# Performance work log

Hardware: AMD Instinct MI355X
Metric: run time of the kernel (lower is better)

The kernel has to match this reference:

```python
import jax, jax.numpy as jnp
import numpy as np

H = 32  # hidden/input size fixed by the module

def _rnn_layer(x, W_ih, b_ih, W_hh, b_hh):
    # x: [B, T, H]. PyTorch RNN: h_t = tanh(x_t @ W_ih^T + b_ih + h_{t-1} @ W_hh^T + b_hh)
    B = x.shape[0]
    # precompute input projection for all timesteps (one big GEMM)
    xin = jnp.einsum('bth,ih->bti', x, W_ih) + (b_ih + b_hh)  # [B, T, H]
    def step(h, xt):
        h_new = jnp.tanh(xt + h @ W_hh.T)
        return h_new, h_new
    h0 = jnp.zeros((B, H), dtype=x.dtype)
    _, hs = jax.lax.scan(step, h0, jnp.swapaxes(xin, 0, 1))  # hs: [T, B, H]
    return jnp.swapaxes(hs, 0, 1)  # [B, T, H]


def setup_inputs() -> dict:
    key = jax.random.key(0)
    ks = jax.random.split(key, 11)
    s = 1.0 / np.sqrt(H)
    u = lambda k, shape: jax.random.uniform(k, shape, jnp.float32, -s, s)
    x = jax.random.normal(ks[0], (4096, 512, H), dtype=jnp.float32)
    return {
        'x': x,
        'W_ih1': u(ks[1], (H, H)), 'W_hh1': u(ks[2], (H, H)),
        'b_ih1': u(ks[3], (H,)),   'b_hh1': u(ks[4], (H,)),
        'W_ih2': u(ks[5], (H, H)), 'W_hh2': u(ks[6], (H, H)),
        'b_ih2': u(ks[7], (H,)),   'b_hh2': u(ks[8], (H,)),
        'W_fc': u(ks[9], (1, H)),  'b_fc': u(ks[10], (1,)),
    }


def reference(x, W_ih1, W_hh1, b_ih1, b_hh1, W_ih2, W_hh2, b_ih2, b_hh2, W_fc, b_fc):
    h1 = _rnn_layer(x, W_ih1, b_ih1, W_hh1, b_hh1)   # [B, T, H]
    h2 = _rnn_layer(h1, W_ih2, b_ih2, W_hh2, b_hh2)  # [B, T, H]
    last = h2[:, -1, :]                               # [B, H]
    return last @ W_fc.T + b_fc                       # [B, 1]
```

## Files before the change

### kernel.cpp

```cpp
#include <hip/hip_runtime.h>

#define HH 32
#define TT 512
#define CHUNK 8
#define NCHUNK (TT / CHUNK)

__device__ __forceinline__ float fast_tanh(float z) {
    float e, r;
    float zz = z * 2.88539008177793f;
    asm("v_exp_f32 %0, %1" : "=v"(e) : "v"(zz));
    float d = e + 1.0f;
    asm("v_rcp_f32 %0, %1" : "=v"(r) : "v"(d));
    return __builtin_fmaf(-2.0f, r, 1.0f);
}

__global__ void __launch_bounds__(64) __attribute__((amdgpu_waves_per_eu(2, 2)))
rnn_fused(
    const float* __restrict__ x,
    const float* __restrict__ Wih1, const float* __restrict__ Whh1,
    const float* __restrict__ bih1, const float* __restrict__ bhh1,
    const float* __restrict__ Wih2, const float* __restrict__ Whh2,
    const float* __restrict__ bih2, const float* __restrict__ bhh2,
    const float* __restrict__ Wfc, const float* __restrict__ bfc,
    float* __restrict__ out)
{
    __shared__ __align__(16) float x_lds[2][CHUNK * HH];
    __shared__ __align__(16) float h1_lds[2][HH];
    __shared__ __align__(16) float h2_lds[2][HH];

    const int lane = threadIdx.x;
    const int g = lane >> 5;
    const int i = lane & 31;
    const int b = blockIdx.x * 2 + g;

    float4 w1[8], u1[8], w2[8], u2[8];
#pragma unroll
    for (int q = 0; q < 8; ++q) {
        w1[q] = ((const float4*)(Wih1 + i * HH))[q];
        u1[q] = ((const float4*)(Whh1 + i * HH))[q];
        w2[q] = ((const float4*)(Wih2 + i * HH))[q];
        u2[q] = ((const float4*)(Whh2 + i * HH))[q];
    }
    const float bias1 = bih1[i] + bhh1[i];
    const float bias2 = bih2[i] + bhh2[i];
    const float wfc = Wfc[i];

    const float* xb = x + (size_t)b * (TT * HH);

    float4 r0 = ((const float4*)xb)[i];
    float4 r1 = ((const float4*)xb)[i + 32];

    float4 h1r[8];
#pragma unroll
    for (int j = 0; j < 8; ++j) h1r[j] = make_float4(0.f, 0.f, 0.f, 0.f);
    float h2_own = 0.0f;
    h2_lds[g][i] = 0.0f;

    float4* xl4 = (float4*)&x_lds[g][0];
    const float4* h1l4 = (const float4*)&h1_lds[g][0];
    const float4* h2l4 = (const float4*)&h2_lds[g][0];

    for (int c = 0; c < NCHUNK; ++c) {
        xl4[i] = r0;
        xl4[i + 32] = r1;
        asm volatile("s_waitcnt lgkmcnt(0)" ::: "memory");
        {
            const int cn = (c + 1 < NCHUNK) ? c + 1 : c;
            const float4* src = (const float4*)(xb + cn * (CHUNK * HH));
            r0 = src[i];
            r1 = src[i + 32];
        }
#pragma unroll
        for (int s = 0; s < CHUNK; ++s) {
            float p0 = bias1, p1 = 0.f, p2 = 0.f, p3 = 0.f;
#pragma unroll
            for (int j = 0; j < 8; ++j) {
                float4 xv = xl4[s * 8 + j];
                p0 = __builtin_fmaf(w1[j].x, xv.x, p0);
                p1 = __builtin_fmaf(w1[j].y, xv.y, p1);
                p2 = __builtin_fmaf(w1[j].z, xv.z, p2);
                p3 = __builtin_fmaf(w1[j].w, xv.w, p3);
            }
#pragma unroll
            for (int j = 0; j < 8; ++j) {
                p0 = __builtin_fmaf(u1[j].x, h1r[j].x, p0);
                p1 = __builtin_fmaf(u1[j].y, h1r[j].y, p1);
                p2 = __builtin_fmaf(u1[j].z, h1r[j].z, p2);
                p3 = __builtin_fmaf(u1[j].w, h1r[j].w, p3);
            }
            float h1n = fast_tanh((p0 + p1) + (p2 + p3));
            h1_lds[g][i] = h1n;
            asm volatile("s_waitcnt lgkmcnt(0)" ::: "memory");

            float q0 = bias2, q1 = 0.f, q2 = 0.f, q3 = 0.f;
#pragma unroll
            for (int j = 0; j < 8; ++j) {
                float4 h1v = h1l4[j];
                float4 h2v = h2l4[j];
                h1r[j] = h1v;
                q0 = __builtin_fmaf(w2[j].x, h1v.x, q0);
                q1 = __builtin_fmaf(w2[j].y, h1v.y, q1);
                q2 = __builtin_fmaf(w2[j].z, h1v.z, q2);
                q3 = __builtin_fmaf(w2[j].w, h1v.w, q3);
                q0 = __builtin_fmaf(u2[j].x, h2v.x, q0);
                q1 = __builtin_fmaf(u2[j].y, h2v.y, q1);
                q2 = __builtin_fmaf(u2[j].z, h2v.z, q2);
                q3 = __builtin_fmaf(u2[j].w, h2v.w, q3);
            }
            float h2n = fast_tanh((q0 + q1) + (q2 + q3));
            h2_own = h2n;
            h2_lds[g][i] = h2n;
        }
    }

    h1_lds[g][i] = h2_own * wfc;
    asm volatile("s_waitcnt lgkmcnt(0)" ::: "memory");
    if (i == 0) {
        float sacc = bfc[0];
#pragma unroll
        for (int j = 0; j < HH; ++j) sacc += h1_lds[g][j];
        out[b] = sacc;
    }
}

extern "C" void kernel_launch(void* const* d_in, const int* in_sizes, int n_in,
                              void* d_out, int out_size, void* d_ws, size_t ws_size,
                              hipStream_t stream) {
    const float* x    = (const float*)d_in[0];
    const float* Wih1 = (const float*)d_in[1];
    const float* Whh1 = (const float*)d_in[2];
    const float* bih1 = (const float*)d_in[3];
    const float* bhh1 = (const float*)d_in[4];
    const float* Wih2 = (const float*)d_in[5];
    const float* Whh2 = (const float*)d_in[6];
    const float* bih2 = (const float*)d_in[7];
    const float* bhh2 = (const float*)d_in[8];
    const float* Wfc  = (const float*)d_in[9];
    const float* bfc  = (const float*)d_in[10];
    float* out = (float*)d_out;

    rnn_fused<<<dim3(2048), dim3(64), 0, stream>>>(
        x, Wih1, Whh1, bih1, bhh1, Wih2, Whh2, bih2, bhh2, Wfc, bfc, out);
}
```

Before: 556.3 us.

## Pipeline RNN layers across wave halves, one batch per block with packed FMAs

Each block now handles a single batch element. The lower 32 lanes compute layer 1 and the upper 32 lanes compute layer 2, one timestep behind, so the two layers run as a skewed pipeline instead of back to back in every lane. Dot products use v_pk_fma_f32 packed math, the weight registers per lane are halved so occupancy can rise (waves_per_eu 4), and the final reduction uses shuffles. The cost is twice as many blocks and a more intricate LDS double-buffer indexing scheme, which adds correctness risk at the chunk boundaries.

```diff
diff --git a/kernel.cpp b/kernel.cpp
--- a/kernel.cpp
+++ b/kernel.cpp
@@ -2,8 +2,26 @@
 
 #define HH 32
 #define TT 512
-#define CHUNK 8
-#define NCHUNK (TT / CHUNK)
+
+typedef float v2f __attribute__((ext_vector_type(2)));
+
+__device__ __forceinline__ v2f pk_fma(v2f a, v2f b, v2f c) {
+    v2f d;
+    asm("v_pk_fma_f32 %0, %1, %2, %3" : "=v"(d) : "v"(a), "v"(b), "v"(c));
+    return d;
+}
+__device__ __forceinline__ v2f pk_mul(v2f a, v2f b) {
+    v2f d;
+    asm("v_pk_mul_f32 %0, %1, %2" : "=v"(d) : "v"(a), "v"(b));
+    return d;
+}
+__device__ __forceinline__ v2f pk_add(v2f a, v2f b) {
+    v2f d;
+    asm("v_pk_add_f32 %0, %1, %2" : "=v"(d) : "v"(a), "v"(b));
+    return d;
+}
+__device__ __forceinline__ v2f flo(float4 v) { return v2f{v.x, v.y}; }
+__device__ __forceinline__ v2f fhi(float4 v) { return v2f{v.z, v.w}; }
 
 __device__ __forceinline__ float fast_tanh(float z) {
     float e, r;
@@ -14,7 +32,7 @@
     return __builtin_fmaf(-2.0f, r, 1.0f);
 }
 
-__global__ void __launch_bounds__(64) __attribute__((amdgpu_waves_per_eu(2, 2)))
+__global__ void __launch_bounds__(64) __attribute__((amdgpu_waves_per_eu(4)))
 rnn_fused(
     const float* __restrict__ x,
     const float* __restrict__ Wih1, const float* __restrict__ Whh1,
@@ -24,103 +42,111 @@
     const float* __restrict__ Wfc, const float* __restrict__ bfc,
     float* __restrict__ out)
 {
-    __shared__ __align__(16) float x_lds[2][CHUNK * HH];
-    __shared__ __align__(16) float h1_lds[2][HH];
-    __shared__ __align__(16) float h2_lds[2][HH];
+    __shared__ __align__(16) float xbuf[2][256];
+    __shared__ __align__(16) float hs[64];
 
     const int lane = threadIdx.x;
-    const int g = lane >> 5;
+    const int half = lane >> 5;
     const int i = lane & 31;
-    const int b = blockIdx.x * 2 + g;
+    const int b = blockIdx.x;
 
-    float4 w1[8], u1[8], w2[8], u2[8];
+    const float* Wp = half ? Wih2 : Wih1;
+    const float* Up = half ? Whh2 : Whh1;
+    v2f wa[16], ub[16];
 #pragma unroll
     for (int q = 0; q < 8; ++q) {
-        w1[q] = ((const float4*)(Wih1 + i * HH))[q];
-        u1[q] = ((const float4*)(Whh1 + i * HH))[q];
-        w2[q] = ((const float4*)(Wih2 + i * HH))[q];
-        u2[q] = ((const float4*)(Whh2 + i * HH))[q];
+        float4 t0 = ((const float4*)(Wp + i * HH))[q];
+        float4 t1 = ((const float4*)(Up + i * HH))[q];
+        wa[2 * q] = flo(t0); wa[2 * q + 1] = fhi(t0);
+        ub[2 * q] = flo(t1); ub[2 * q + 1] = fhi(t1);
     }
-    const float bias1 = bih1[i] + bhh1[i];
-    const float bias2 = bih2[i] + bhh2[i];
-    const float wfc = Wfc[i];
+    const float* bip = half ? bih2 : bih1;
+    const float* bhp = half ? bhh2 : bhh1;
+    const float bias = bip[i] + bhp[i];
 
-    const float* xb = x + (size_t)b * (TT * HH);
+    const float4* xb4 = (const float4*)(x + (size_t)b * (TT * HH));
 
-    float4 r0 = ((const float4*)xb)[i];
-    float4 r1 = ((const float4*)xb)[i + 32];
+    char* xbase = (char*)&xbuf[0][0];
+    const char* Abase = half ? (const char*)&hs[0] : (const char*)xbase;
+    const unsigned maskA = half ? 0u : 0xFFFFFFFFu;
+    const float4* Bp = (const float4*)(half ? &hs[32] : &hs[0]);
 
-    float4 h1r[8];
+    hs[lane] = 0.0f;
+    float4 r = xb4[lane];
+    ((float4*)xbase)[lane] = r;
+    r = xb4[64 + lane];
+    asm volatile("s_waitcnt lgkmcnt(0)" ::: "memory");
+
+    float last = 0.0f;
+
+    auto phase = [&](unsigned xoff, bool zero_upper) {
+        const float4* Ap = (const float4*)(Abase + (xoff & maskA));
+        float4 a0 = Ap[0], a1 = Ap[1], a2 = Ap[2], a3 = Ap[3];
+        v2f c0 = pk_mul(wa[0], flo(a0));
+        v2f c1 = pk_mul(wa[1], fhi(a0));
+        v2f c2 = pk_mul(wa[2], flo(a1));
+        v2f c3 = pk_mul(wa[3], fhi(a1));
+        float4 a4 = Ap[4], a5 = Ap[5], a6 = Ap[6], a7 = Ap[7];
+        c0 = pk_fma(wa[4], flo(a2), c0);
+        c1 = pk_fma(wa[5], fhi(a2), c1);
+        c2 = pk_fma(wa[6], flo(a3), c2);
+        c3 = pk_fma(wa[7], fhi(a3), c3);
+        c0 = pk_fma(wa[8], flo(a4), c0);
+        c1 = pk_fma(wa[9], fhi(a4), c1);
+        c2 = pk_fma(wa[10], flo(a5), c2);
+        c3 = pk_fma(wa[11], fhi(a5), c3);
+        c0 = pk_fma(wa[12], flo(a6), c0);
+        c1 = pk_fma(wa[13], fhi(a6), c1);
+        c2 = pk_fma(wa[14], flo(a7), c2);
+        c3 = pk_fma(wa[15], fhi(a7), c3);
+        float4 b0 = Bp[0], b1 = Bp[1], b2 = Bp[2], b3 = Bp[3];
+        c0 = pk_fma(ub[0], flo(b0), c0);
+        c1 = pk_fma(ub[1], fhi(b0), c1);
+        c2 = pk_fma(ub[2], flo(b1), c2);
+        c3 = pk_fma(ub[3], fhi(b1), c3);
+        float4 b4 = Bp[4], b5 = Bp[5], b6 = Bp[6], b7 = Bp[7];
+        c0 = pk_fma(ub[4], flo(b2), c0);
+        c1 = pk_fma(ub[5], fhi(b2), c1);
+        c2 = pk_fma(ub[6], flo(b3), c2);
+        c3 = pk_fma(ub[7], fhi(b3), c3);
+        c0 = pk_fma(ub[8], flo(b4), c0);
+        c1 = pk_fma(ub[9], fhi(b4), c1);
+        c2 = pk_fma(ub[10], flo(b5), c2);
+        c3 = pk_fma(ub[11], fhi(b5), c3);
+        c0 = pk_fma(ub[12], flo(b6), c0);
+        c1 = pk_fma(ub[13], fhi(b6), c1);
+        c2 = pk_fma(ub[14], flo(b7), c2);
+        c3 = pk_fma(ub[15], fhi(b7), c3);
+        v2f s = pk_add(pk_add(c0, c1), pk_add(c2, c3));
+        float h = fast_tanh((s.x + s.y) + bias);
+        if (zero_upper && half) h = 0.0f;
+        hs[lane] = h;
+        asm volatile("s_waitcnt lgkmcnt(0)" ::: "memory");
+        return h;
+    };
+
+    last = phase(0u, true);
+
+#pragma unroll 2
+    for (int c = 0; c < 64; ++c) {
+        ((float4*)(xbase + ((c + 1) & 1) * 1024))[lane] = r;
+        int cn = (c + 2 <= 63) ? (c + 2) : 63;
+        r = xb4[cn * 64 + lane];
 #pragma unroll
-    for (int j = 0; j < 8; ++j) h1r[j] = make_float4(0.f, 0.f, 0.f, 0.f);
-    float h2_own = 0.0f;
-    h2_lds[g][i] = 0.0f;
-
-    float4* xl4 = (float4*)&x_lds[g][0];
-    const float4* h1l4 = (const float4*)&h1_lds[g][0];
-    const float4* h2l4 = (const float4*)&h2_lds[g][0];
-
-    for (int c = 0; c < NCHUNK; ++c) {
-        xl4[i] = r0;
-        xl4[i + 32] = r1;
-        asm volatile("s_waitcnt lgkmcnt(0)" ::: "memory");
-        {
-            const int cn = (c + 1 < NCHUNK) ? c + 1 : c;
-            const float4* src = (const float4*)(xb + cn * (CHUNK * HH));
-            r0 = src[i];
-            r1 = src[i + 32];
-        }
-#pragma unroll
-        for (int s = 0; s < CHUNK; ++s) {
-            float p0 = bias1, p1 = 0.f, p2 = 0.f, p3 = 0.f;
-#pragma unroll
-            for (int j = 0; j < 8; ++j) {
-                float4 xv = xl4[s * 8 + j];
-                p0 = __builtin_fmaf(w1[j].x, xv.x, p0);
-                p1 = __builtin_fmaf(w1[j].y, xv.y, p1);
-                p2 = __builtin_fmaf(w1[j].z, xv.z, p2);
-                p3 = __builtin_fmaf(w1[j].w, xv.w, p3);
-            }
-#pragma unroll
-            for (int j = 0; j < 8; ++j) {
-                p0 = __builtin_fmaf(u1[j].x, h1r[j].x, p0);
-                p1 = __builtin_fmaf(u1[j].y, h1r[j].y, p1);
-                p2 = __builtin_fmaf(u1[j].z, h1r[j].z, p2);
-                p3 = __builtin_fmaf(u1[j].w, h1r[j].w, p3);
-            }
-            float h1n = fast_tanh((p0 + p1) + (p2 + p3));
-            h1_lds[g][i] = h1n;
-            asm volatile("s_waitcnt lgkmcnt(0)" ::: "memory");
-
-            float q0 = bias2, q1 = 0.f, q2 = 0.f, q3 = 0.f;
-#pragma unroll
-            for (int j = 0; j < 8; ++j) {
-                float4 h1v = h1l4[j];
-                float4 h2v = h2l4[j];
-                h1r[j] = h1v;
-                q0 = __builtin_fmaf(w2[j].x, h1v.x, q0);
-                q1 = __builtin_fmaf(w2[j].y, h1v.y, q1);
-                q2 = __builtin_fmaf(w2[j].z, h1v.z, q2);
-                q3 = __builtin_fmaf(w2[j].w, h1v.w, q3);
-                q0 = __builtin_fmaf(u2[j].x, h2v.x, q0);
-                q1 = __builtin_fmaf(u2[j].y, h2v.y, q1);
-                q2 = __builtin_fmaf(u2[j].z, h2v.z, q2);
-                q3 = __builtin_fmaf(u2[j].w, h2v.w, q3);
-            }
-            float h2n = fast_tanh((q0 + q1) + (q2 + q3));
-            h2_own = h2n;
-            h2_lds[g][i] = h2n;
+        for (int s = 0; s < 8; ++s) {
+            unsigned slot = (unsigned)((s + 1) & 7);
+            unsigned par = (s < 7) ? (unsigned)(c & 1) : (unsigned)((c + 1) & 1);
+            last = phase(par * 1024u + slot * 128u, false);
         }
     }
 
-    h1_lds[g][i] = h2_own * wfc;
-    asm volatile("s_waitcnt lgkmcnt(0)" ::: "memory");
-    if (i == 0) {
-        float sacc = bfc[0];
-#pragma unroll
-        for (int j = 0; j < HH; ++j) sacc += h1_lds[g][j];
-        out[b] = sacc;
-    }
+    float rr = last * Wfc[i];
+    rr += __shfl_xor(rr, 1);
+    rr += __shfl_xor(rr, 2);
+    rr += __shfl_xor(rr, 4);
+    rr += __shfl_xor(rr, 8);
+    rr += __shfl_xor(rr, 16);
+    if (lane == 32) out[b] = rr + bfc[0];
 }
 
 extern "C" void kernel_launch(void* const* d_in, const int* in_sizes, int n_in,
@@ -139,6 +165,6 @@
     const float* bfc  = (const float*)d_in[10];
     float* out = (float*)d_out;
 
-    rnn_fused<<<dim3(2048), dim3(64), 0, stream>>>(
+    rnn_fused<<<dim3(4096), dim3(64), 0, stream>>>(
         x, Wih1, Whh1, bih1, bhh1, Wih2, Whh2, bih2, bhh2, Wfc, bfc, out);
 }
```

Result: slower. 716.9 us (+28.9%).
